# Kernel optimization log

Hardware: AMD Instinct MI355X
Metric: run time of the kernel (lower is better)

## Reference

```python
import jax, jax.numpy as jnp
import numpy as np

BATCH = 8192
FEAT_DIM = 768
MULTIPLE_CONVEX = 4
NUM_CONVEX = BATCH * MULTIPLE_CONVEX
NUM_LABELS = 150
UNSEEN_LABEL_ID = 150


def setup_inputs() -> dict:
    key = jax.random.key(0)
    k_z, k_s = jax.random.split(key)
    z = jax.random.normal(k_z, (BATCH, FEAT_DIM), dtype=jnp.float32)
    s = jax.random.uniform(k_s, (NUM_CONVEX,), dtype=jnp.float32)

    # Host-side rejection sampling of index pairs with distinct labels,
    # mirroring the original np.random.choice-until-labels-differ loop.
    rng = np.random.default_rng(0)
    labels = rng.integers(0, NUM_LABELS, size=BATCH)
    idx_i = rng.integers(0, BATCH, size=NUM_CONVEX)
    idx_j = rng.integers(0, BATCH, size=NUM_CONVEX)
    bad = labels[idx_i] == labels[idx_j]
    while bad.any():
        idx_j[bad] = rng.integers(0, BATCH, size=int(bad.sum()))
        bad = labels[idx_i] == labels[idx_j]

    return {
        "z": z,
        "label_ids": jnp.asarray(labels, dtype=jnp.int64 if jax.config.jax_enable_x64 else jnp.int32),
        "idx_i": jnp.asarray(idx_i, dtype=jnp.int32),
        "idx_j": jnp.asarray(idx_j, dtype=jnp.int32),
        "s": s,
    }


def reference(z, label_ids, idx_i, idx_j, s):
    # convex[k] = s[k] * z[i_k] + (1 - s[k]) * z[j_k]  -- gather + axpy
    sw = s[:, None]  # [NUM_CONVEX, 1]
    convex = sw * z[idx_i] + (1.0 - sw) * z[idx_j]  # [NUM_CONVEX, FEAT_DIM]
    z_out = jnp.concatenate([z, convex], axis=0)  # [BATCH+NUM_CONVEX, FEAT_DIM]
    unseen = jnp.full((idx_i.shape[0],), UNSEEN_LABEL_ID, dtype=label_ids.dtype)
    labels_out = jnp.concatenate([label_ids, unseen], axis=0)
    return z_out, labels_out
```

## Files before the change

### kernel.cpp

```cpp
#include <hip/hip_runtime.h>
#include <stdint.h>

#define BATCH 8192
#define FEAT 768
#define NCVX 32768
#define NOUT (BATCH + NCVX)
#define UNSEEN 150

typedef float f32x4 __attribute__((ext_vector_type(4)));

#define ROW_CHUNKS (FEAT / 4)
constexpr int COPY_CHUNKS = BATCH * ROW_CHUNKS;
constexpr int CVX_CHUNKS  = NCVX  * ROW_CHUNKS;
constexpr int LAB_CHUNKS  = NOUT / 4;
constexpr int TOTAL_CHUNKS = COPY_CHUNKS + CVX_CHUNKS + LAB_CHUNKS;

__global__ __launch_bounds__(256) void ConvexSampler_39006892982339_kernel(
    const float* __restrict__ z,
    const int*   __restrict__ labels,
    const int*   __restrict__ idx_i,
    const int*   __restrict__ idx_j,
    const float* __restrict__ s,
    float*       __restrict__ out)
{
    int t = blockIdx.x * 256 + threadIdx.x;
    if (t >= TOTAL_CHUNKS) return;

    if (t < COPY_CHUNKS) {
        f32x4 v = ((const f32x4*)z)[t];
        __builtin_nontemporal_store(v, &((f32x4*)out)[t]);
    } else if (t < COPY_CHUNKS + CVX_CHUNKS) {
        int c   = t - COPY_CHUNKS;
        int row = c / ROW_CHUNKS;
        int col = c - row * ROW_CHUNKS;
        float sw  = s[row];
        float sw1 = 1.0f - sw;
        const f32x4* ap = (const f32x4*)(z + (size_t)idx_i[row] * FEAT) + col;
        const f32x4* bp = (const f32x4*)(z + (size_t)idx_j[row] * FEAT) + col;
        f32x4 a = *ap;
        f32x4 b = *bp;
        f32x4 r = sw * a + sw1 * b;
        __builtin_nontemporal_store(r, &((f32x4*)out)[t]);
    } else {
        int c    = t - (COPY_CHUNKS + CVX_CHUNKS);
        int base = c * 4;
        f32x4 r;
        r.x = (float)(base + 0 < BATCH ? labels[base + 0] : UNSEEN);
        r.y = (float)(base + 1 < BATCH ? labels[base + 1] : UNSEEN);
        r.z = (float)(base + 2 < BATCH ? labels[base + 2] : UNSEEN);
        r.w = (float)(base + 3 < BATCH ? labels[base + 3] : UNSEEN);
        __builtin_nontemporal_store(r, &((f32x4*)(out + (size_t)NOUT * FEAT))[c]);
    }
}

extern "C" void kernel_launch(void* const* d_in, const int* in_sizes, int n_in,
                              void* d_out, int out_size, void* d_ws, size_t ws_size,
                              hipStream_t stream) {
    const float* z      = (const float*)d_in[0];
    const int*   labels = (const int*)d_in[1];
    const int*   idx_i  = (const int*)d_in[2];
    const int*   idx_j  = (const int*)d_in[3];
    const float* s      = (const float*)d_in[4];
    float*       out    = (float*)d_out;

    int blocks = (TOTAL_CHUNKS + 255) / 256;
    ConvexSampler_39006892982339_kernel<<<blocks, 256, 0, stream>>>(
        z, labels, idx_i, idx_j, s, out);
}
```

Baseline: 173.7 us.

## Use persistent grid-stride kernel with one wave per convex row

Replaces the one-thread-per-chunk launch with a fixed grid of 2048 blocks. Each thread copies several z chunks, and each wave computes whole convex rows with three vector loads per lane from each source row. This removes per-thread division and repeated index/s loads, and it issues more independent loads per thread. The trade-off is fewer resident waves and serial row iteration, which may reduce latency hiding.

```diff
diff --git a/kernel.cpp b/kernel.cpp
--- a/kernel.cpp
+++ b/kernel.cpp
@@ -11,9 +11,11 @@
 
 #define ROW_CHUNKS (FEAT / 4)
 constexpr int COPY_CHUNKS = BATCH * ROW_CHUNKS;
-constexpr int CVX_CHUNKS  = NCVX  * ROW_CHUNKS;
 constexpr int LAB_CHUNKS  = NOUT / 4;
-constexpr int TOTAL_CHUNKS = COPY_CHUNKS + CVX_CHUNKS + LAB_CHUNKS;
+
+constexpr int BLOCKS   = 2048;
+constexpr int NTHREADS = BLOCKS * 256;
+constexpr int NWAVES   = NTHREADS / 64;
 
 __global__ __launch_bounds__(256) void ConvexSampler_39006892982339_kernel(
     const float* __restrict__ z,
@@ -23,33 +25,45 @@
     const float* __restrict__ s,
     float*       __restrict__ out)
 {
-    int t = blockIdx.x * 256 + threadIdx.x;
-    if (t >= TOTAL_CHUNKS) return;
+    const int tid  = blockIdx.x * 256 + threadIdx.x;
+    const int lane = threadIdx.x & 63;
+    const int wid  = tid >> 6;
 
-    if (t < COPY_CHUNKS) {
-        f32x4 v = ((const f32x4*)z)[t];
-        __builtin_nontemporal_store(v, &((f32x4*)out)[t]);
-    } else if (t < COPY_CHUNKS + CVX_CHUNKS) {
-        int c   = t - COPY_CHUNKS;
-        int row = c / ROW_CHUNKS;
-        int col = c - row * ROW_CHUNKS;
+    const f32x4* z4   = (const f32x4*)z;
+    f32x4*       out4 = (f32x4*)out;
+
+    #pragma unroll
+    for (int it = 0; it < COPY_CHUNKS / NTHREADS; ++it) {
+        int c = tid + it * NTHREADS;
+        __builtin_nontemporal_store(z4[c], &out4[c]);
+    }
+
+    for (int row = wid; row < NCVX; row += NWAVES) {
         float sw  = s[row];
         float sw1 = 1.0f - sw;
-        const f32x4* ap = (const f32x4*)(z + (size_t)idx_i[row] * FEAT) + col;
-        const f32x4* bp = (const f32x4*)(z + (size_t)idx_j[row] * FEAT) + col;
-        f32x4 a = *ap;
-        f32x4 b = *bp;
-        f32x4 r = sw * a + sw1 * b;
-        __builtin_nontemporal_store(r, &((f32x4*)out)[t]);
-    } else {
-        int c    = t - (COPY_CHUNKS + CVX_CHUNKS);
-        int base = c * 4;
+        const f32x4* ap = z4 + (size_t)idx_i[row] * ROW_CHUNKS;
+        const f32x4* bp = z4 + (size_t)idx_j[row] * ROW_CHUNKS;
+        f32x4*       op = out4 + COPY_CHUNKS + (size_t)row * ROW_CHUNKS;
+
+        f32x4 a0 = ap[lane];
+        f32x4 a1 = ap[lane + 64];
+        f32x4 a2 = ap[lane + 128];
+        f32x4 b0 = bp[lane];
+        f32x4 b1 = bp[lane + 64];
+        f32x4 b2 = bp[lane + 128];
+        __builtin_nontemporal_store(sw * a0 + sw1 * b0, &op[lane]);
+        __builtin_nontemporal_store(sw * a1 + sw1 * b1, &op[lane + 64]);
+        __builtin_nontemporal_store(sw * a2 + sw1 * b2, &op[lane + 128]);
+    }
+
+    if (tid < LAB_CHUNKS) {
+        int base = tid * 4;
         f32x4 r;
         r.x = (float)(base + 0 < BATCH ? labels[base + 0] : UNSEEN);
         r.y = (float)(base + 1 < BATCH ? labels[base + 1] : UNSEEN);
         r.z = (float)(base + 2 < BATCH ? labels[base + 2] : UNSEEN);
         r.w = (float)(base + 3 < BATCH ? labels[base + 3] : UNSEEN);
-        __builtin_nontemporal_store(r, &((f32x4*)(out + (size_t)NOUT * FEAT))[c]);
+        __builtin_nontemporal_store(r, &((f32x4*)(out + (size_t)NOUT * FEAT))[tid]);
     }
 }
 
@@ -63,7 +77,6 @@
     const float* s      = (const float*)d_in[4];
     float*       out    = (float*)d_out;
 
-    int blocks = (TOTAL_CHUNKS + 255) / 256;
-    ConvexSampler_39006892982339_kernel<<<blocks, 256, 0, stream>>>(
+    ConvexSampler_39006892982339_kernel<<<BLOCKS, 256, 0, stream>>>(
         z, labels, idx_i, idx_j, s, out);
 }
```

Measured after the change: 173.9 us. No clear change (+0.1%).
